# Optimization experiments

Measured on AMD Instinct MI355X. Metric: run time of the kernel, lower is better.

## Reference

```python
import jax, jax.numpy as jnp
import numpy as np

EPS = 1e-6


def setup_inputs() -> dict:
    key = jax.random.key(0)
    k1, k2, k3 = jax.random.split(key, 3)
    B, N1, N2, D, K, C = 8, 1024, 1024, 1, 5, 3
    xa = jax.random.normal(k1, (B, N1, D, C), dtype=jnp.float32)
    features = jax.random.normal(k2, (B, N1, K, C), dtype=jnp.float32)
    xt = jax.random.normal(k3, (B, N2, D, C), dtype=jnp.float32)
    # learned parameter: log_std of shape (in_dims, num_basis, num_channels)
    log_std = jnp.log(1e-6 + 0.1 * jnp.ones((D, K, C), dtype=jnp.float32))
    return {"xa": xa, "features": features, "xt": xt, "log_std": log_std}


def reference(xa, features, xt, log_std):
    # xa: (B, N1, D, C), xt: (B, N2, D, C), features: (B, N1, K, C), log_std: (D, K, C)
    std = jnp.exp(log_std) + EPS                       # (D, K, C)
    x1 = xa[:, :, :, None, :] / std                    # (B, N1, D, K, C)
    x2 = xt[:, :, :, None, :] / std                    # (B, N2, D, K, C)
    sq1 = jnp.sum(x1 * x1, axis=2)                     # (B, N1, K, C)
    sq2 = jnp.sum(x2 * x2, axis=2)                     # (B, N2, K, C)
    # pairwise squared distance per basis/channel
    prod = jnp.einsum('bndkc,bmdkc->bnmkc', x1, x2)    # (B, N1, N2, K, C)
    dist = sq1[:, :, None] + sq2[:, None] - 2.0 * prod # (B, N1, N2, K, C)
    wt = jnp.exp(-0.5 * dist)                          # RBF weights
    # weighted sum over context points N1
    smoothed = jnp.einsum('bnkc,bnmkc->bmkc', features, wt)  # (B, N2, K, C)
    return smoothed
```

## Files before the change

### kernel.cpp

```cpp
#include <hip/hip_runtime.h>

#define EPS_F 1e-6f
#define LOG2E 1.4426950408889634f

typedef float f4a __attribute__((ext_vector_type(4), aligned(16)));

__device__ __forceinline__ float rfl(float x) {
    return __builtin_bit_cast(float, __builtin_amdgcn_readfirstlane(__builtin_bit_cast(int, x)));
}

__global__ __launch_bounds__(256, 8) void icgp_partial_kernel(
    const float* __restrict__ xa,
    const float* __restrict__ feat,
    const float* __restrict__ xt,
    const float* __restrict__ log_std,
    float* __restrict__ pws)
{
    __shared__ float lds[3840];

    const int bid  = blockIdx.x;
    const int nsb  = bid & 15;
    const int mt   = (bid >> 4) & 15;
    const int b    = bid >> 8;
    const int tid  = threadIdx.x;
    const int wv   = tid >> 6;
    const int lane = tid & 63;
    const int m    = mt * 64 + lane;
    const int n0   = nsb * 64;

    const float* __restrict__ fg = feat + ((size_t)b * 1024 + n0) * 15;
    if (tid < 240) {
        const f4a v = *(const f4a*)(fg + tid * 4);
        #pragma unroll
        for (int e = 0; e < 4; ++e) {
            const int g = tid * 4 + e;
            const int r = g / 15, c = g - r * 15;
            lds[r * 16 + c] = v[e];
        }
    }
    const float* __restrict__ ag = xa + ((size_t)b * 1024 + n0) * 3;
    if (tid < 48) {
        const f4a v = *(const f4a*)(ag + tid * 4);
        #pragma unroll
        for (int e = 0; e < 4; ++e) {
            const int g = tid * 4 + e;
            const int r = g / 3, c = g - r * 3;
            lds[1024 + r * 4 + c] = v[e];
        }
    }

    float coef[15];
    #pragma unroll
    for (int kc = 0; kc < 15; ++kc) {
        const float s = __expf(log_std[kc]) + EPS_F;
        coef[kc] = rfl(-0.5f * LOG2E / (s * s));
    }
    bool uni = true;
    #pragma unroll
    for (int k = 1; k < 5; ++k)
        #pragma unroll
        for (int c = 0; c < 3; ++c)
            uni = uni && (coef[k * 3 + c] == coef[c]);

    const float t0 = xt[(b * 1024 + m) * 3 + 0];
    const float t1 = xt[(b * 1024 + m) * 3 + 1];
    const float t2 = xt[(b * 1024 + m) * 3 + 2];

    __syncthreads();

    float acc[15];
    #pragma unroll
    for (int kc = 0; kc < 15; ++kc) acc[kc] = 0.0f;

    const int rb = wv * 16;

    if (uni) {
        const float c0 = coef[0], c1 = coef[1], c2 = coef[2];
        #pragma unroll 2
        for (int i = 0; i < 16; ++i) {
            const float* __restrict__ row = &lds[(rb + i) * 16];
            const f4a fA = *(const f4a*)(row);
            const f4a fB = *(const f4a*)(row + 4);
            const f4a fC = *(const f4a*)(row + 8);
            const f4a fD = *(const f4a*)(row + 12);
            const f4a av = *(const f4a*)(&lds[1024 + (rb + i) * 4]);
            float d0 = av.x - t0; d0 *= d0;
            float d1 = av.y - t1; d1 *= d1;
            float d2 = av.z - t2; d2 *= d2;
            const float w0 = __builtin_amdgcn_exp2f(d0 * c0);
            const float w1 = __builtin_amdgcn_exp2f(d1 * c1);
            const float w2 = __builtin_amdgcn_exp2f(d2 * c2);
            acc[0]  += w0 * fA.x;  acc[1]  += w1 * fA.y;  acc[2]  += w2 * fA.z;
            acc[3]  += w0 * fA.w;  acc[4]  += w1 * fB.x;  acc[5]  += w2 * fB.y;
            acc[6]  += w0 * fB.z;  acc[7]  += w1 * fB.w;  acc[8]  += w2 * fC.x;
            acc[9]  += w0 * fC.y;  acc[10] += w1 * fC.z;  acc[11] += w2 * fC.w;
            acc[12] += w0 * fD.x;  acc[13] += w1 * fD.y;  acc[14] += w2 * fD.z;
        }
    } else {
        for (int i = 0; i < 16; ++i) {
            const float* __restrict__ row = &lds[(rb + i) * 16];
            float fv[16];
            *(f4a*)(fv)      = *(const f4a*)(row);
            *(f4a*)(fv + 4)  = *(const f4a*)(row + 4);
            *(f4a*)(fv + 8)  = *(const f4a*)(row + 8);
            *(f4a*)(fv + 12) = *(const f4a*)(row + 12);
            const f4a av = *(const f4a*)(&lds[1024 + (rb + i) * 4]);
            float dd[3];
            dd[0] = av.x - t0; dd[0] *= dd[0];
            dd[1] = av.y - t1; dd[1] *= dd[1];
            dd[2] = av.z - t2; dd[2] *= dd[2];
            #pragma unroll
            for (int k = 0; k < 5; ++k)
                #pragma unroll
                for (int c = 0; c < 3; ++c)
                    acc[k * 3 + c] +=
                        __builtin_amdgcn_exp2f(dd[c] * coef[k * 3 + c]) * fv[k * 3 + c];
        }
    }

    __syncthreads();
    #pragma unroll
    for (int kc = 0; kc < 15; ++kc) lds[tid * 15 + kc] = acc[kc];
    __syncthreads();

    float* __restrict__ pb = pws + (size_t)nsb * 122880
                                 + ((size_t)b * 1024 + mt * 64) * 15;
    #pragma unroll
    for (int j = 0; j < 4; ++j) {
        const int o = j * 256 + tid;
        if (o < 960) {
            const int mm = o / 15, kc = o - mm * 15;
            float s = 0.0f;
            #pragma unroll
            for (int w = 0; w < 4; ++w)
                s += lds[(w * 64 + mm) * 15 + kc];
            pb[o] = s;
        }
    }
}

__global__ __launch_bounds__(256) void icgp_reduce_kernel(
    const float* __restrict__ pws, float* __restrict__ out)
{
    const int idx = blockIdx.x * 256 + threadIdx.x;
    f4a s = {0.0f, 0.0f, 0.0f, 0.0f};
    #pragma unroll
    for (int ns = 0; ns < 16; ++ns) {
        const f4a v = *(const f4a*)(pws + (size_t)ns * 122880 + idx * 4);
        s.x += v.x; s.y += v.y; s.z += v.z; s.w += v.w;
    }
    *(f4a*)(out + idx * 4) = s;
}

extern "C" void kernel_launch(void* const* d_in, const int* in_sizes, int n_in,
                              void* d_out, int out_size, void* d_ws, size_t ws_size,
                              hipStream_t stream) {
    const float* xa      = (const float*)d_in[0];
    const float* feat    = (const float*)d_in[1];
    const float* xt      = (const float*)d_in[2];
    const float* log_std = (const float*)d_in[3];
    float* out = (float*)d_out;
    float* pws = (float*)d_ws;

    icgp_partial_kernel<<<dim3(2048), dim3(256), 0, stream>>>(xa, feat, xt, log_std, pws);
    icgp_reduce_kernel<<<dim3(120), dim3(256), 0, stream>>>(pws, out);
}
```

Baseline: 77.05 us.

## Read context rows directly from global memory, halve N-splits, precompute coefficients

Drops the LDS staging of features and context positions. Each wave now reads its rows straight from global memory through wave-uniform (scalar-friendly) addresses. The N dimension is split into 8 chunks of 128 rows instead of 16 chunks of 64, which halves the partial workspace and the reduce work. The per-block exp/divide for the coefficients moves into a separate one-thread kernel. This removes a barrier and the LDS stores, but adds a third kernel launch and relies on scalar loads and caches for the features.

```diff
diff --git a/kernel.cpp b/kernel.cpp
--- a/kernel.cpp
+++ b/kernel.cpp
@@ -5,125 +5,108 @@
 
 typedef float f4a __attribute__((ext_vector_type(4), aligned(16)));
 
-__device__ __forceinline__ float rfl(float x) {
-    return __builtin_bit_cast(float, __builtin_amdgcn_readfirstlane(__builtin_bit_cast(int, x)));
+__global__ void icgp_coef_kernel(const float* __restrict__ log_std,
+                                 float* __restrict__ cb) {
+    if (threadIdx.x == 0) {
+        float c[15];
+        #pragma unroll
+        for (int kc = 0; kc < 15; ++kc) {
+            const float s = __expf(log_std[kc]) + EPS_F;
+            c[kc] = -0.5f * LOG2E / (s * s);
+        }
+        bool uni = true;
+        #pragma unroll
+        for (int k = 1; k < 5; ++k)
+            #pragma unroll
+            for (int ch = 0; ch < 3; ++ch)
+                uni = uni && (c[k * 3 + ch] == c[ch]);
+        #pragma unroll
+        for (int kc = 0; kc < 15; ++kc) cb[kc] = c[kc];
+        cb[15] = uni ? 1.0f : 0.0f;
+    }
 }
 
-__global__ __launch_bounds__(256, 8) void icgp_partial_kernel(
+__global__ __launch_bounds__(256, 4) void icgp_partial_kernel(
     const float* __restrict__ xa,
     const float* __restrict__ feat,
     const float* __restrict__ xt,
-    const float* __restrict__ log_std,
+    const float* __restrict__ cb,
     float* __restrict__ pws)
 {
     __shared__ float lds[3840];
 
     const int bid  = blockIdx.x;
-    const int nsb  = bid & 15;
-    const int mt   = (bid >> 4) & 15;
-    const int b    = bid >> 8;
+    const int nc   = bid & 7;
+    const int mt   = (bid >> 3) & 15;
+    const int b    = bid >> 7;
     const int tid  = threadIdx.x;
     const int wv   = tid >> 6;
     const int lane = tid & 63;
     const int m    = mt * 64 + lane;
-    const int n0   = nsb * 64;
-
-    const float* __restrict__ fg = feat + ((size_t)b * 1024 + n0) * 15;
-    if (tid < 240) {
-        const f4a v = *(const f4a*)(fg + tid * 4);
-        #pragma unroll
-        for (int e = 0; e < 4; ++e) {
-            const int g = tid * 4 + e;
-            const int r = g / 15, c = g - r * 15;
-            lds[r * 16 + c] = v[e];
-        }
-    }
-    const float* __restrict__ ag = xa + ((size_t)b * 1024 + n0) * 3;
-    if (tid < 48) {
-        const f4a v = *(const f4a*)(ag + tid * 4);
-        #pragma unroll
-        for (int e = 0; e < 4; ++e) {
-            const int g = tid * 4 + e;
-            const int r = g / 3, c = g - r * 3;
-            lds[1024 + r * 4 + c] = v[e];
-        }
-    }
 
     float coef[15];
     #pragma unroll
-    for (int kc = 0; kc < 15; ++kc) {
-        const float s = __expf(log_std[kc]) + EPS_F;
-        coef[kc] = rfl(-0.5f * LOG2E / (s * s));
-    }
-    bool uni = true;
-    #pragma unroll
-    for (int k = 1; k < 5; ++k)
-        #pragma unroll
-        for (int c = 0; c < 3; ++c)
-            uni = uni && (coef[k * 3 + c] == coef[c]);
+    for (int kc = 0; kc < 15; ++kc) coef[kc] = cb[kc];
+    const bool uni = (cb[15] != 0.0f);
 
     const float t0 = xt[(b * 1024 + m) * 3 + 0];
     const float t1 = xt[(b * 1024 + m) * 3 + 1];
     const float t2 = xt[(b * 1024 + m) * 3 + 2];
 
-    __syncthreads();
+    const int rw = __builtin_amdgcn_readfirstlane(nc * 128 + wv * 32);
+    const float* __restrict__ fg = feat + (size_t)b * 1024 * 15;
+    const float* __restrict__ ag = xa   + (size_t)b * 1024 * 3;
 
     float acc[15];
     #pragma unroll
     for (int kc = 0; kc < 15; ++kc) acc[kc] = 0.0f;
 
-    const int rb = wv * 16;
-
     if (uni) {
         const float c0 = coef[0], c1 = coef[1], c2 = coef[2];
-        #pragma unroll 2
-        for (int i = 0; i < 16; ++i) {
-            const float* __restrict__ row = &lds[(rb + i) * 16];
-            const f4a fA = *(const f4a*)(row);
-            const f4a fB = *(const f4a*)(row + 4);
-            const f4a fC = *(const f4a*)(row + 8);
-            const f4a fD = *(const f4a*)(row + 12);
-            const f4a av = *(const f4a*)(&lds[1024 + (rb + i) * 4]);
-            float d0 = av.x - t0; d0 *= d0;
-            float d1 = av.y - t1; d1 *= d1;
-            float d2 = av.z - t2; d2 *= d2;
+        #pragma unroll 4
+        for (int i = 0; i < 32; ++i) {
+            const int r = rw + i;
+            const float* __restrict__ f = fg + r * 15;
+            const float a0 = ag[r * 3 + 0];
+            const float a1 = ag[r * 3 + 1];
+            const float a2 = ag[r * 3 + 2];
+            float d0 = a0 - t0; d0 *= d0;
+            float d1 = a1 - t1; d1 *= d1;
+            float d2 = a2 - t2; d2 *= d2;
             const float w0 = __builtin_amdgcn_exp2f(d0 * c0);
             const float w1 = __builtin_amdgcn_exp2f(d1 * c1);
             const float w2 = __builtin_amdgcn_exp2f(d2 * c2);
-            acc[0]  += w0 * fA.x;  acc[1]  += w1 * fA.y;  acc[2]  += w2 * fA.z;
-            acc[3]  += w0 * fA.w;  acc[4]  += w1 * fB.x;  acc[5]  += w2 * fB.y;
-            acc[6]  += w0 * fB.z;  acc[7]  += w1 * fB.w;  acc[8]  += w2 * fC.x;
-            acc[9]  += w0 * fC.y;  acc[10] += w1 * fC.z;  acc[11] += w2 * fC.w;
-            acc[12] += w0 * fD.x;  acc[13] += w1 * fD.y;  acc[14] += w2 * fD.z;
+            acc[0]  += w0 * f[0];   acc[1]  += w1 * f[1];   acc[2]  += w2 * f[2];
+            acc[3]  += w0 * f[3];   acc[4]  += w1 * f[4];   acc[5]  += w2 * f[5];
+            acc[6]  += w0 * f[6];   acc[7]  += w1 * f[7];   acc[8]  += w2 * f[8];
+            acc[9]  += w0 * f[9];   acc[10] += w1 * f[10];  acc[11] += w2 * f[11];
+            acc[12] += w0 * f[12];  acc[13] += w1 * f[13];  acc[14] += w2 * f[14];
         }
     } else {
-        for (int i = 0; i < 16; ++i) {
-            const float* __restrict__ row = &lds[(rb + i) * 16];
-            float fv[16];
-            *(f4a*)(fv)      = *(const f4a*)(row);
-            *(f4a*)(fv + 4)  = *(const f4a*)(row + 4);
-            *(f4a*)(fv + 8)  = *(const f4a*)(row + 8);
-            *(f4a*)(fv + 12) = *(const f4a*)(row + 12);
-            const f4a av = *(const f4a*)(&lds[1024 + (rb + i) * 4]);
+        for (int i = 0; i < 32; ++i) {
+            const int r = rw + i;
+            const float* __restrict__ f = fg + r * 15;
+            const float a0 = ag[r * 3 + 0];
+            const float a1 = ag[r * 3 + 1];
+            const float a2 = ag[r * 3 + 2];
             float dd[3];
-            dd[0] = av.x - t0; dd[0] *= dd[0];
-            dd[1] = av.y - t1; dd[1] *= dd[1];
-            dd[2] = av.z - t2; dd[2] *= dd[2];
+            dd[0] = a0 - t0; dd[0] *= dd[0];
+            dd[1] = a1 - t1; dd[1] *= dd[1];
+            dd[2] = a2 - t2; dd[2] *= dd[2];
             #pragma unroll
             for (int k = 0; k < 5; ++k)
                 #pragma unroll
                 for (int c = 0; c < 3; ++c)
                     acc[k * 3 + c] +=
-                        __builtin_amdgcn_exp2f(dd[c] * coef[k * 3 + c]) * fv[k * 3 + c];
+                        __builtin_amdgcn_exp2f(dd[c] * coef[k * 3 + c]) * f[k * 3 + c];
         }
     }
 
-    __syncthreads();
     #pragma unroll
     for (int kc = 0; kc < 15; ++kc) lds[tid * 15 + kc] = acc[kc];
     __syncthreads();
 
-    float* __restrict__ pb = pws + (size_t)nsb * 122880
+    float* __restrict__ pb = pws + (size_t)nc * 122880
                                  + ((size_t)b * 1024 + mt * 64) * 15;
     #pragma unroll
     for (int j = 0; j < 4; ++j) {
@@ -145,7 +128,7 @@
     const int idx = blockIdx.x * 256 + threadIdx.x;
     f4a s = {0.0f, 0.0f, 0.0f, 0.0f};
     #pragma unroll
-    for (int ns = 0; ns < 16; ++ns) {
+    for (int ns = 0; ns < 8; ++ns) {
         const f4a v = *(const f4a*)(pws + (size_t)ns * 122880 + idx * 4);
         s.x += v.x; s.y += v.y; s.z += v.z; s.w += v.w;
     }
@@ -161,7 +144,9 @@
     const float* log_std = (const float*)d_in[3];
     float* out = (float*)d_out;
     float* pws = (float*)d_ws;
+    float* cb  = pws + 8 * 122880;
 
-    icgp_partial_kernel<<<dim3(2048), dim3(256), 0, stream>>>(xa, feat, xt, log_std, pws);
+    icgp_coef_kernel<<<dim3(1), dim3(64), 0, stream>>>(log_std, cb);
+    icgp_partial_kernel<<<dim3(1024), dim3(256), 0, stream>>>(xa, feat, xt, cb, pws);
     icgp_reduce_kernel<<<dim3(120), dim3(256), 0, stream>>>(pws, out);
 }
```

New measurement: 74.29 us. 1.04x faster.
